# Performance work log

Measured on AMD Instinct MI355X. Metric: run time of the kernel, lower is better.

The kernel has to match this reference:

```python
import jax, jax.numpy as jnp
import numpy as np

B, T, F, H, L = 128, 256, 1024, 1024, 2

def setup_inputs() -> dict:
    key = jax.random.key(0)
    ks = jax.random.split(key, 9)
    s_in = 1.0 / np.sqrt(F)
    s_h = 1.0 / np.sqrt(H)
    return {
        "x": jax.random.normal(ks[0], (B, T, F), jnp.float32),
        "W_ih0": jax.random.normal(ks[1], (4 * H, F), jnp.float32) * s_in,
        "b_ih0": jax.random.normal(ks[2], (4 * H,), jnp.float32) * s_in,
        "W_hh0": jax.random.normal(ks[3], (4 * H, H), jnp.float32) * s_h,
        "b_hh0": jax.random.normal(ks[4], (4 * H,), jnp.float32) * s_h,
        "W_ih1": jax.random.normal(ks[5], (4 * H, H), jnp.float32) * s_h,
        "b_ih1": jax.random.normal(ks[6], (4 * H,), jnp.float32) * s_h,
        "W_hh1": jax.random.normal(ks[7], (4 * H, H), jnp.float32) * s_h,
        "b_hh1": jax.random.normal(ks[8], (4 * H,), jnp.float32) * s_h,
    }

def _cell(x_t, h, c, W_ih, b_ih, W_hh, b_hh):
    # gates: (B, 4H); chunk order i, f, g, o (matches torch .chunk(4, dim=1))
    gates = x_t @ W_ih.T + b_ih + h @ W_hh.T + b_hh
    i, f, g, o = jnp.split(gates, 4, axis=1)
    i = jax.nn.sigmoid(i)
    f = jax.nn.sigmoid(f)
    g = jnp.tanh(g)
    o = jax.nn.sigmoid(o)
    c_new = f * c + i * g
    h_new = o * jnp.tanh(c_new)
    return h_new, c_new

def reference(x, W_ih0, b_ih0, W_hh0, b_hh0, W_ih1, b_ih1, W_hh1, b_hh1):
    Bv = x.shape[0]
    z = jnp.zeros((Bv, H), x.dtype)
    init = (z, z, z, z)  # h0, c0, h1, c1

    def step(carry, x_t):
        h0, c0, h1, c1 = carry
        h0, c0 = _cell(x_t, h0, c0, W_ih0, b_ih0, W_hh0, b_hh0)
        h1, c1 = _cell(h0, h1, c1, W_ih1, b_ih1, W_hh1, b_hh1)
        return (h0, c0, h1, c1), h1

    # scan over time: xs shaped (T, B, F)
    _, ys = jax.lax.scan(step, init, jnp.swapaxes(x, 0, 1))
    return jnp.swapaxes(ys, 0, 1)  # (B, T, H)
```

## Files before the change

### kernel.cpp

```cpp
#include <hip/hip_runtime.h>

#define B_ 128
#define T_ 256
#define F_ 1024
#define H_ 1024

typedef __bf16 bf16x8 __attribute__((ext_vector_type(8)));
typedef __bf16 bf16x4 __attribute__((ext_vector_type(4)));
typedef float f32x4 __attribute__((ext_vector_type(4)));

#define WROW 2056

__device__ __forceinline__ float sigf(float v)  { return 1.0f / (1.0f + __expf(-v)); }
__device__ __forceinline__ float tanhfast(float x) { return 1.0f - 2.0f / (1.0f + __expf(2.0f * x)); }

__global__ void k_cvt(const float* __restrict__ src, __bf16* __restrict__ dst, int n) {
    int i = (blockIdx.x * 256 + threadIdx.x) * 8;
    if (i + 7 < n) {
        float4 a = *(const float4*)(src + i);
        float4 b = *(const float4*)(src + i + 4);
        bf16x8 o = { (__bf16)a.x, (__bf16)a.y, (__bf16)a.z, (__bf16)a.w,
                     (__bf16)b.x, (__bf16)b.y, (__bf16)b.z, (__bf16)b.w };
        *(bf16x8*)(dst + i) = o;
    }
}

__global__ void k_init(__bf16* h0b, __bf16* h1b, unsigned* bar) {
    int i = blockIdx.x * 256 + threadIdx.x;
    h0b[i] = (__bf16)0.0f;
    h1b[i] = (__bf16)0.0f;
    if (i < 64) bar[i] = 0u;
}

#define STEP(A0, A1, KW) do { \
    bf16x8 b0_ = *(const bf16x8*)&wB[lrow][(KW) + quad * 8]; \
    bf16x8 b1_ = *(const bf16x8*)&wB[16 + lrow][(KW) + quad * 8]; \
    acc00 = __builtin_amdgcn_mfma_f32_16x16x32_bf16(A0, b0_, acc00, 0, 0, 0); \
    acc01 = __builtin_amdgcn_mfma_f32_16x16x32_bf16(A0, b1_, acc01, 0, 0, 0); \
    acc10 = __builtin_amdgcn_mfma_f32_16x16x32_bf16(A1, b0_, acc10, 0, 0, 0); \
    acc11 = __builtin_amdgcn_mfma_f32_16x16x32_bf16(A1, b1_, acc11, 0, 0, 0); \
} while (0)

#define KLOOP_BF16(SRC, STRIDE, WBASE) do { \
    const __bf16* pa_ = (SRC) + (long)arow0 * (STRIDE) + kbase + quad * 8; \
    const __bf16* pb_ = (SRC) + (long)arow1 * (STRIDE) + kbase + quad * 8; \
    _Pragma("unroll 8") \
    for (int ks_ = 0; ks_ < 16; ++ks_) { \
        bf16x8 a0_ = *(const bf16x8*)(pa_ + ks_ * 32); \
        bf16x8 a1_ = *(const bf16x8*)(pb_ + ks_ * 32); \
        STEP(a0_, a1_, (WBASE) + kbase + ks_ * 32); \
    } \
} while (0)

#define KLOOP_F32(SRC, STRIDE, WBASE) do { \
    const float* pa_ = (SRC) + (long)arow0 * (STRIDE) + kbase + quad * 8; \
    const float* pb_ = (SRC) + (long)arow1 * (STRIDE) + kbase + quad * 8; \
    _Pragma("unroll 4") \
    for (int ks_ = 0; ks_ < 16; ++ks_) { \
        float4 va_ = *(const float4*)(pa_ + ks_ * 32); \
        float4 vb_ = *(const float4*)(pa_ + ks_ * 32 + 4); \
        float4 vc_ = *(const float4*)(pb_ + ks_ * 32); \
        float4 vd_ = *(const float4*)(pb_ + ks_ * 32 + 4); \
        bf16x8 a0_ = { (__bf16)va_.x, (__bf16)va_.y, (__bf16)va_.z, (__bf16)va_.w, \
                       (__bf16)vb_.x, (__bf16)vb_.y, (__bf16)vb_.z, (__bf16)vb_.w }; \
        bf16x8 a1_ = { (__bf16)vc_.x, (__bf16)vc_.y, (__bf16)vc_.z, (__bf16)vc_.w, \
                       (__bf16)vd_.x, (__bf16)vd_.y, (__bf16)vd_.z, (__bf16)vd_.w }; \
        STEP(a0_, a1_, (WBASE) + kbase + ks_ * 32); \
    } \
} while (0)

#define ZACC() do { \
    acc00 = (f32x4){0.f,0.f,0.f,0.f}; acc01 = (f32x4){0.f,0.f,0.f,0.f}; \
    acc10 = (f32x4){0.f,0.f,0.f,0.f}; acc11 = (f32x4){0.f,0.f,0.f,0.f}; \
} while (0)

#define EPI(MT, ACC_A, ACC_B, HW, TT, WOUT) \
    _Pragma("unroll") \
    for (int r = 0; r < 4; ++r) { \
        float v0 = (ACC_A)[r], v1 = (ACC_B)[r]; \
        float q0 = __shfl_xor(v0, 8); \
        float q1 = __shfl_xor(v1, 8); \
        float iv = (hi ? q0 : v0) + bi; \
        float fv = (hi ? v0 : q0) + bf_; \
        float gv = (hi ? q1 : v1) + bg; \
        float ov = (hi ? v1 : q1) + bo; \
        float cn = sigf(fv) * creg[MT][r] + sigf(iv) * tanhfast(gv); \
        creg[MT][r] = cn; \
        float hn = sigf(ov) * tanhfast(cn); \
        if (!hi) { \
            const int b = (wave << 5) + (MT) * 16 + (quad << 2) + r; \
            (HW)[(long)b * H_ + j0 + jj] = (__bf16)hn; \
            if (WOUT) out[((long)b * T_ + (TT)) * H_ + j0 + jj] = hn; \
        } \
    }

#define REDUCE_EPI(HW, TT, WOUT) do { \
    if (wave >= 4) { \
        red[wave - 4][lane][0] = acc00; red[wave - 4][lane][1] = acc01; \
        red[wave - 4][lane][2] = acc10; red[wave - 4][lane][3] = acc11; \
    } \
    __syncthreads(); \
    if (wave < 4) { \
        acc00 += red[wave][lane][0]; acc01 += red[wave][lane][1]; \
        acc10 += red[wave][lane][2]; acc11 += red[wave][lane][3]; \
        const float bi  = bb[jj]; \
        const float bf_ = bb[8 + jj]; \
        const float bg  = bb[16 + jj]; \
        const float bo  = bb[24 + jj]; \
        EPI(0, acc00, acc01, HW, TT, WOUT); \
        EPI(1, acc10, acc11, HW, TT, WOUT); \
    } \
} while (0)

__global__ __launch_bounds__(512, 2) void lstm_persist(
    const float* __restrict__ x,
    const float* __restrict__ Wih0, const float* __restrict__ Whh0,
    const float* __restrict__ Wih1, const float* __restrict__ Whh1,
    const float* __restrict__ bih0, const float* __restrict__ bhh0,
    const float* __restrict__ bih1, const float* __restrict__ bhh1,
    __bf16* __restrict__ h0a, __bf16* __restrict__ h0b,
    __bf16* __restrict__ h1a, __bf16* __restrict__ h1b,
    unsigned* bar, const __bf16* __restrict__ xb, float* __restrict__ out)
{
    const int cell = blockIdx.x >> 7;
    const int cidx = blockIdx.x & 127;
    const int j0   = cidx << 3;

    __shared__ __align__(16) __bf16 wB[32][WROW];
    __shared__ __align__(16) f32x4  red[4][64][4];
    __shared__ float bb[32];

    const int tid  = threadIdx.x;
    const int wave = tid >> 6;
    const int lane = tid & 63;
    const int quad = lane >> 4;
    const int lrow = lane & 15;
    const int jj   = lane & 7;
    const bool hi  = (lane & 8) != 0;

    const int kbase = (wave >> 2) << 9;
    const int arow0 = ((wave & 3) << 5) + lrow;
    const int arow1 = arow0 + 16;

    unsigned* cnt = bar;
    unsigned* gen = bar + 32;

    const float* Wih = cell ? Wih1 : Wih0;
    const float* Whh = cell ? Whh1 : Whh0;

    for (int e = tid; e < 32 * 512; e += 512) {
        int n  = e >> 9;
        int k  = (e & 511) << 2;
        int wr = ((n >> 3) << 10) + j0 + (n & 7);
        const float* src = (k < 1024) ? (Wih + (long)wr * 1024 + k)
                                      : (Whh + (long)wr * 1024 + (k - 1024));
        float4 v = *(const float4*)src;
        bf16x4 o = { (__bf16)v.x, (__bf16)v.y, (__bf16)v.z, (__bf16)v.w };
        *(bf16x4*)&wB[n][k] = o;
    }
    if (tid < 32) {
        int wr = ((tid >> 3) << 10) + j0 + (tid & 7);
        bb[tid] = cell ? (bih1[wr] + bhh1[wr]) : (bih0[wr] + bhh0[wr]);
    }
    __syncthreads();

    float creg[2][4] = {};
    f32x4 acc00, acc01, acc10, acc11;
    ZACC();

    if (cell == 0) {
        if (xb) KLOOP_BF16(xb + 0, (long)T_ * F_, 0);
        else    KLOOP_F32 (x  + 0, (long)T_ * F_, 0);
    }

    for (int p = 0; p <= T_; ++p) {
        if (cell == 0) {
            if (p < T_) {
                const int t = p;
                const __bf16* hprev = (t & 1) ? h0a : h0b;
                __bf16* hw          = (t & 1) ? h0b : h0a;
                KLOOP_BF16(hprev, H_, 1024);
                REDUCE_EPI(hw, t, false);
            }
        } else {
            if (p >= 1) {
                const int t = p - 1;
                ZACC();
                const __bf16* s0 = (t & 1) ? h0b : h0a;
                const __bf16* s1 = (t & 1) ? h1a : h1b;
                __bf16* hw       = (t & 1) ? h1b : h1a;
                KLOOP_BF16(s0, H_, 0);
                KLOOP_BF16(s1, H_, 1024);
                REDUCE_EPI(hw, t, true);
            }
        }

        if (p < T_) {
            __syncthreads();
            unsigned g = 0;
            if (tid == 0) {
                __threadfence();
                g = __hip_atomic_load(gen, __ATOMIC_RELAXED, __HIP_MEMORY_SCOPE_AGENT);
                unsigned a = __hip_atomic_fetch_add(cnt, 1u, __ATOMIC_RELAXED,
                                                    __HIP_MEMORY_SCOPE_AGENT);
                if (a == 255u) {
                    __hip_atomic_store(cnt, 0u, __ATOMIC_RELAXED, __HIP_MEMORY_SCOPE_AGENT);
                    __hip_atomic_store(gen, g + 1u, __ATOMIC_RELEASE, __HIP_MEMORY_SCOPE_AGENT);
                }
            }
            if (cell == 0) {
                ZACC();
                if (p + 1 < T_) {
                    if (xb) KLOOP_BF16(xb + (long)(p + 1) * F_, (long)T_ * F_, 0);
                    else    KLOOP_F32 (x  + (long)(p + 1) * F_, (long)T_ * F_, 0);
                }
            }
            if (tid == 0) {
                for (;;) {
                    bool done = false;
                    for (int it = 0; it < 256; ++it) {
                        if (__hip_atomic_load(gen, __ATOMIC_RELAXED,
                                              __HIP_MEMORY_SCOPE_AGENT) != g) { done = true; break; }
                        __builtin_amdgcn_s_sleep(2);
                    }
                    if (done) break;
                    if (__hip_atomic_load(gen, __ATOMIC_ACQUIRE,
                                          __HIP_MEMORY_SCOPE_AGENT) != g) break;
                }
                __builtin_amdgcn_fence(__ATOMIC_ACQUIRE, "agent");
            }
            __syncthreads();
        }
    }
}

extern "C" void kernel_launch(void* const* d_in, const int* in_sizes, int n_in,
                              void* d_out, int out_size, void* d_ws, size_t ws_size,
                              hipStream_t stream)
{
    const float* x    = (const float*)d_in[0];
    const float* Wih0 = (const float*)d_in[1];
    const float* bih0 = (const float*)d_in[2];
    const float* Whh0 = (const float*)d_in[3];
    const float* bhh0 = (const float*)d_in[4];
    const float* Wih1 = (const float*)d_in[5];
    const float* bih1 = (const float*)d_in[6];
    const float* Whh1 = (const float*)d_in[7];
    const float* bhh1 = (const float*)d_in[8];
    float* out = (float*)d_out;

    char* ws = (char*)d_ws;
    unsigned* bar = (unsigned*)ws;
    __bf16* h0a = (__bf16*)(ws + 4096);
    __bf16* h0b = (__bf16*)(ws + 4096 + (256 << 10));
    __bf16* h1a = (__bf16*)(ws + 4096 + (512 << 10));
    __bf16* h1b = (__bf16*)(ws + 4096 + (768 << 10));
    const __bf16* xb = nullptr;

    const size_t XB_OFF = 4096 + (1 << 20);
    if (ws_size >= XB_OFF + ((size_t)64 << 20)) {
        __bf16* xbw = (__bf16*)(ws + XB_OFF);
        k_cvt<<<dim3(16384), dim3(256), 0, stream>>>(x, xbw, B_ * T_ * F_);
        xb = xbw;
    }
    k_init<<<dim3(512), dim3(256), 0, stream>>>(h0b, h1b, bar);

    void* args[] = {
        (void*)&x, (void*)&Wih0, (void*)&Whh0, (void*)&Wih1, (void*)&Whh1,
        (void*)&bih0, (void*)&bhh0, (void*)&bih1, (void*)&bhh1,
        (void*)&h0a, (void*)&h0b, (void*)&h1a, (void*)&h1b,
        (void*)&bar, (void*)&xb, (void*)&out
    };
    hipError_t err = hipLaunchCooperativeKernel((const void*)lstm_persist,
                                                dim3(256), dim3(512), args, 0, stream);
    if (err != hipSuccess) {
        lstm_persist<<<dim3(256), dim3(512), 0, stream>>>(
            x, Wih0, Whh0, Wih1, Whh1, bih0, bhh0, bih1, bhh1,
            h0a, h0b, h1a, h1b, bar, xb, out);
    }
    (void)in_sizes; (void)n_in; (void)out_size;
}
```

Measured before the change: 7.381 ms.

## Software-pipeline A-operand loads in K loops and transpose reduction buffer layout

Each K loop now preloads the A-operand rows (hidden state or x) into a register ring buffer and issues the load for a later step while the MFMAs for the current step run. The goal is to hide global-memory latency on the recurrent critical path. The cross-wave reduction buffer is changed from f32x4-per-lane to a scalar layout indexed [element][lane], which should avoid LDS bank conflicts. Launch bounds drop from 2 to 1 wave-group per SIMD to leave room for the extra registers, which lowers possible occupancy, though one persistent block per CU may already be the case.

```diff
diff --git a/kernel.cpp b/kernel.cpp
--- a/kernel.cpp
+++ b/kernel.cpp
@@ -44,10 +44,20 @@
 #define KLOOP_BF16(SRC, STRIDE, WBASE) do { \
     const __bf16* pa_ = (SRC) + (long)arow0 * (STRIDE) + kbase + quad * 8; \
     const __bf16* pb_ = (SRC) + (long)arow1 * (STRIDE) + kbase + quad * 8; \
-    _Pragma("unroll 8") \
+    bf16x8 ra_[8], rb_[8]; \
+    _Pragma("unroll") \
+    for (int i_ = 0; i_ < 8; ++i_) { \
+        ra_[i_] = *(const bf16x8*)(pa_ + i_ * 32); \
+        rb_[i_] = *(const bf16x8*)(pb_ + i_ * 32); \
+    } \
+    _Pragma("unroll") \
     for (int ks_ = 0; ks_ < 16; ++ks_) { \
-        bf16x8 a0_ = *(const bf16x8*)(pa_ + ks_ * 32); \
-        bf16x8 a1_ = *(const bf16x8*)(pb_ + ks_ * 32); \
+        bf16x8 a0_ = ra_[ks_ & 7]; \
+        bf16x8 a1_ = rb_[ks_ & 7]; \
+        if (ks_ < 8) { \
+            ra_[ks_ & 7] = *(const bf16x8*)(pa_ + (ks_ + 8) * 32); \
+            rb_[ks_ & 7] = *(const bf16x8*)(pb_ + (ks_ + 8) * 32); \
+        } \
         STEP(a0_, a1_, (WBASE) + kbase + ks_ * 32); \
     } \
 } while (0)
@@ -55,12 +65,24 @@
 #define KLOOP_F32(SRC, STRIDE, WBASE) do { \
     const float* pa_ = (SRC) + (long)arow0 * (STRIDE) + kbase + quad * 8; \
     const float* pb_ = (SRC) + (long)arow1 * (STRIDE) + kbase + quad * 8; \
-    _Pragma("unroll 4") \
+    float4 rA_[4], rB_[4], rC_[4], rD_[4]; \
+    _Pragma("unroll") \
+    for (int i_ = 0; i_ < 4; ++i_) { \
+        rA_[i_] = *(const float4*)(pa_ + i_ * 32); \
+        rB_[i_] = *(const float4*)(pa_ + i_ * 32 + 4); \
+        rC_[i_] = *(const float4*)(pb_ + i_ * 32); \
+        rD_[i_] = *(const float4*)(pb_ + i_ * 32 + 4); \
+    } \
+    _Pragma("unroll") \
     for (int ks_ = 0; ks_ < 16; ++ks_) { \
-        float4 va_ = *(const float4*)(pa_ + ks_ * 32); \
-        float4 vb_ = *(const float4*)(pa_ + ks_ * 32 + 4); \
-        float4 vc_ = *(const float4*)(pb_ + ks_ * 32); \
-        float4 vd_ = *(const float4*)(pb_ + ks_ * 32 + 4); \
+        float4 va_ = rA_[ks_ & 3], vb_ = rB_[ks_ & 3]; \
+        float4 vc_ = rC_[ks_ & 3], vd_ = rD_[ks_ & 3]; \
+        if (ks_ < 12) { \
+            rA_[ks_ & 3] = *(const float4*)(pa_ + (ks_ + 4) * 32); \
+            rB_[ks_ & 3] = *(const float4*)(pa_ + (ks_ + 4) * 32 + 4); \
+            rC_[ks_ & 3] = *(const float4*)(pb_ + (ks_ + 4) * 32); \
+            rD_[ks_ & 3] = *(const float4*)(pb_ + (ks_ + 4) * 32 + 4); \
+        } \
         bf16x8 a0_ = { (__bf16)va_.x, (__bf16)va_.y, (__bf16)va_.z, (__bf16)va_.w, \
                        (__bf16)vb_.x, (__bf16)vb_.y, (__bf16)vb_.z, (__bf16)vb_.w }; \
         bf16x8 a1_ = { (__bf16)vc_.x, (__bf16)vc_.y, (__bf16)vc_.z, (__bf16)vc_.w, \
@@ -96,13 +118,23 @@
 
 #define REDUCE_EPI(HW, TT, WOUT) do { \
     if (wave >= 4) { \
-        red[wave - 4][lane][0] = acc00; red[wave - 4][lane][1] = acc01; \
-        red[wave - 4][lane][2] = acc10; red[wave - 4][lane][3] = acc11; \
+        _Pragma("unroll") \
+        for (int i_ = 0; i_ < 4; ++i_) { \
+            red[wave - 4][i_     ][lane] = acc00[i_]; \
+            red[wave - 4][i_ + 4 ][lane] = acc01[i_]; \
+            red[wave - 4][i_ + 8 ][lane] = acc10[i_]; \
+            red[wave - 4][i_ + 12][lane] = acc11[i_]; \
+        } \
     } \
     __syncthreads(); \
     if (wave < 4) { \
-        acc00 += red[wave][lane][0]; acc01 += red[wave][lane][1]; \
-        acc10 += red[wave][lane][2]; acc11 += red[wave][lane][3]; \
+        _Pragma("unroll") \
+        for (int i_ = 0; i_ < 4; ++i_) { \
+            acc00[i_] += red[wave][i_     ][lane]; \
+            acc01[i_] += red[wave][i_ + 4 ][lane]; \
+            acc10[i_] += red[wave][i_ + 8 ][lane]; \
+            acc11[i_] += red[wave][i_ + 12][lane]; \
+        } \
         const float bi  = bb[jj]; \
         const float bf_ = bb[8 + jj]; \
         const float bg  = bb[16 + jj]; \
@@ -112,7 +144,7 @@
     } \
 } while (0)
 
-__global__ __launch_bounds__(512, 2) void lstm_persist(
+__global__ __launch_bounds__(512, 1) void lstm_persist(
     const float* __restrict__ x,
     const float* __restrict__ Wih0, const float* __restrict__ Whh0,
     const float* __restrict__ Wih1, const float* __restrict__ Whh1,
@@ -127,7 +159,7 @@
     const int j0   = cidx << 3;
 
     __shared__ __align__(16) __bf16 wB[32][WROW];
-    __shared__ __align__(16) f32x4  red[4][64][4];
+    __shared__ __align__(16) float  red[4][16][64];
     __shared__ float bb[32];
 
     const int tid  = threadIdx.x;
```

Measured after the change: 7.376 ms. Within noise of the previous version (-0.1%).

## Replace global barrier with per-cell hierarchical counters and multi-slot hidden state buffers

Applied to the files above, without the earlier changes.

Replaces the single grid-wide barrier per timestep with a two-level (leaf/root) counter tree per layer and per-layer generation flags. Consumers wait only on the specific layer state they need, so layer 0 and layer 1 can run skewed in a wavefront pipeline. Hidden states go into time-indexed slots (all T slots if the workspace is large, otherwise a 4-slot ring with back-pressure) stored in a k-blocked layout for coalesced loads. The K split across waves changes from halves of one matrix to x-part versus h-part. The reduction scratch is transposed, and launch bounds drop to one block per CU. It adds memory-ordering complexity and relies on spin-waits being correct.

```diff
diff --git a/kernel.cpp b/kernel.cpp
--- a/kernel.cpp
+++ b/kernel.cpp
@@ -10,6 +10,7 @@
 typedef float f32x4 __attribute__((ext_vector_type(4)));
 
 #define WROW 2056
+#define HSLOT 131072L
 
 __device__ __forceinline__ float sigf(float v)  { return 1.0f / (1.0f + __expf(-v)); }
 __device__ __forceinline__ float tanhfast(float x) { return 1.0f - 2.0f / (1.0f + __expf(2.0f * x)); }
@@ -25,12 +26,20 @@
     }
 }
 
-__global__ void k_init(__bf16* h0b, __bf16* h1b, unsigned* bar) {
+__global__ void k_init(__bf16* h0s, __bf16* h1s, unsigned* bar) {
     int i = blockIdx.x * 256 + threadIdx.x;
-    h0b[i] = (__bf16)0.0f;
-    h1b[i] = (__bf16)0.0f;
-    if (i < 64) bar[i] = 0u;
-}
+    h0s[i] = (__bf16)0.0f;
+    h1s[i] = (__bf16)0.0f;
+    if (i < 512) bar[i] = 0u;
+}
+
+#define WAITGE(P, V) do { \
+    while (__hip_atomic_load((P), __ATOMIC_RELAXED, __HIP_MEMORY_SCOPE_AGENT) < (V)) \
+        __builtin_amdgcn_s_sleep(1); \
+    asm volatile("" ::: "memory"); \
+} while (0)
+
+#define ACQ() __builtin_amdgcn_fence(__ATOMIC_ACQUIRE, "agent")
 
 #define STEP(A0, A1, KW) do { \
     bf16x8 b0_ = *(const bf16x8*)&wB[lrow][(KW) + quad * 8]; \
@@ -41,22 +50,32 @@
     acc11 = __builtin_amdgcn_mfma_f32_16x16x32_bf16(A1, b1_, acc11, 0, 0, 0); \
 } while (0)
 
-#define KLOOP_BF16(SRC, STRIDE, WBASE) do { \
-    const __bf16* pa_ = (SRC) + (long)arow0 * (STRIDE) + kbase + quad * 8; \
-    const __bf16* pb_ = (SRC) + (long)arow1 * (STRIDE) + kbase + quad * 8; \
-    _Pragma("unroll 8") \
-    for (int ks_ = 0; ks_ < 16; ++ks_) { \
+#define KLOOP_HF(SRC, WBASE) do { \
+    const __bf16* ph_ = (SRC) + (long)quad * 1024 + arow0 * 8; \
+    _Pragma("unroll") \
+    for (int ks_ = 0; ks_ < 32; ++ks_) { \
+        bf16x8 a0_ = *(const bf16x8*)(ph_ + (long)ks_ * 4096); \
+        bf16x8 a1_ = *(const bf16x8*)(ph_ + (long)ks_ * 4096 + 128); \
+        STEP(a0_, a1_, (WBASE) + ks_ * 32); \
+    } \
+} while (0)
+
+#define KLOOP_RMF(SRC, S, WBASE) do { \
+    const __bf16* pa_ = (SRC) + (long)arow0 * (S) + quad * 8; \
+    const __bf16* pb_ = (SRC) + (long)arow1 * (S) + quad * 8; \
+    _Pragma("unroll") \
+    for (int ks_ = 0; ks_ < 32; ++ks_) { \
         bf16x8 a0_ = *(const bf16x8*)(pa_ + ks_ * 32); \
         bf16x8 a1_ = *(const bf16x8*)(pb_ + ks_ * 32); \
-        STEP(a0_, a1_, (WBASE) + kbase + ks_ * 32); \
-    } \
-} while (0)
-
-#define KLOOP_F32(SRC, STRIDE, WBASE) do { \
-    const float* pa_ = (SRC) + (long)arow0 * (STRIDE) + kbase + quad * 8; \
-    const float* pb_ = (SRC) + (long)arow1 * (STRIDE) + kbase + quad * 8; \
-    _Pragma("unroll 4") \
-    for (int ks_ = 0; ks_ < 16; ++ks_) { \
+        STEP(a0_, a1_, (WBASE) + ks_ * 32); \
+    } \
+} while (0)
+
+#define KLOOP_F32F(SRC, S, WBASE) do { \
+    const float* pa_ = (SRC) + (long)arow0 * (S) + quad * 8; \
+    const float* pb_ = (SRC) + (long)arow1 * (S) + quad * 8; \
+    _Pragma("unroll") \
+    for (int ks_ = 0; ks_ < 32; ++ks_) { \
         float4 va_ = *(const float4*)(pa_ + ks_ * 32); \
         float4 vb_ = *(const float4*)(pa_ + ks_ * 32 + 4); \
         float4 vc_ = *(const float4*)(pb_ + ks_ * 32); \
@@ -65,7 +84,7 @@
                        (__bf16)vb_.x, (__bf16)vb_.y, (__bf16)vb_.z, (__bf16)vb_.w }; \
         bf16x8 a1_ = { (__bf16)vc_.x, (__bf16)vc_.y, (__bf16)vc_.z, (__bf16)vc_.w, \
                        (__bf16)vd_.x, (__bf16)vd_.y, (__bf16)vd_.z, (__bf16)vd_.w }; \
-        STEP(a0_, a1_, (WBASE) + kbase + ks_ * 32); \
+        STEP(a0_, a1_, (WBASE) + ks_ * 32); \
     } \
 } while (0)
 
@@ -89,20 +108,30 @@
         float hn = sigf(ov) * tanhfast(cn); \
         if (!hi) { \
             const int b = (wave << 5) + (MT) * 16 + (quad << 2) + r; \
-            (HW)[(long)b * H_ + j0 + jj] = (__bf16)hn; \
+            (HW)[b * 8 + jj] = (__bf16)hn; \
             if (WOUT) out[((long)b * T_ + (TT)) * H_ + j0 + jj] = hn; \
         } \
     }
 
 #define REDUCE_EPI(HW, TT, WOUT) do { \
     if (wave >= 4) { \
-        red[wave - 4][lane][0] = acc00; red[wave - 4][lane][1] = acc01; \
-        red[wave - 4][lane][2] = acc10; red[wave - 4][lane][3] = acc11; \
+        _Pragma("unroll") \
+        for (int i_ = 0; i_ < 4; ++i_) { \
+            red[wave - 4][i_     ][lane] = acc00[i_]; \
+            red[wave - 4][i_ + 4 ][lane] = acc01[i_]; \
+            red[wave - 4][i_ + 8 ][lane] = acc10[i_]; \
+            red[wave - 4][i_ + 12][lane] = acc11[i_]; \
+        } \
     } \
     __syncthreads(); \
     if (wave < 4) { \
-        acc00 += red[wave][lane][0]; acc01 += red[wave][lane][1]; \
-        acc10 += red[wave][lane][2]; acc11 += red[wave][lane][3]; \
+        _Pragma("unroll") \
+        for (int i_ = 0; i_ < 4; ++i_) { \
+            acc00[i_] += red[wave][i_     ][lane]; \
+            acc01[i_] += red[wave][i_ + 4 ][lane]; \
+            acc10[i_] += red[wave][i_ + 8 ][lane]; \
+            acc11[i_] += red[wave][i_ + 12][lane]; \
+        } \
         const float bi  = bb[jj]; \
         const float bf_ = bb[8 + jj]; \
         const float bg  = bb[16 + jj]; \
@@ -112,22 +141,22 @@
     } \
 } while (0)
 
-__global__ __launch_bounds__(512, 2) void lstm_persist(
+__global__ __launch_bounds__(512, 1) void lstm_persist(
     const float* __restrict__ x,
     const float* __restrict__ Wih0, const float* __restrict__ Whh0,
     const float* __restrict__ Wih1, const float* __restrict__ Whh1,
     const float* __restrict__ bih0, const float* __restrict__ bhh0,
     const float* __restrict__ bih1, const float* __restrict__ bhh1,
-    __bf16* __restrict__ h0a, __bf16* __restrict__ h0b,
-    __bf16* __restrict__ h1a, __bf16* __restrict__ h1b,
-    unsigned* bar, const __bf16* __restrict__ xb, float* __restrict__ out)
+    __bf16* __restrict__ h0s, __bf16* __restrict__ h1s,
+    unsigned* bar, const __bf16* __restrict__ xb,
+    float* __restrict__ out, int big)
 {
     const int cell = blockIdx.x >> 7;
     const int cidx = blockIdx.x & 127;
     const int j0   = cidx << 3;
 
     __shared__ __align__(16) __bf16 wB[32][WROW];
-    __shared__ __align__(16) f32x4  red[4][64][4];
+    __shared__ __align__(16) float  red[4][16][64];
     __shared__ float bb[32];
 
     const int tid  = threadIdx.x;
@@ -138,12 +167,14 @@
     const int jj   = lane & 7;
     const bool hi  = (lane & 8) != 0;
 
-    const int kbase = (wave >> 2) << 9;
     const int arow0 = ((wave & 3) << 5) + lrow;
     const int arow1 = arow0 + 16;
 
-    unsigned* cnt = bar;
-    unsigned* gen = bar + 32;
+    unsigned* leaf = bar + (cell ? 160 : 0) + ((cidx & 7) << 4);
+    unsigned* root = bar + (cell ? 288 : 128);
+    unsigned* genA = bar + 144;
+    unsigned* genB = bar + 304;
+    unsigned* genMy = cell ? genB : genA;
 
     const float* Wih = cell ? Wih1 : Wih0;
     const float* Whh = cell ? Whh1 : Whh0;
@@ -166,70 +197,50 @@
 
     float creg[2][4] = {};
     f32x4 acc00, acc01, acc10, acc11;
-    ZACC();
-
-    if (cell == 0) {
-        if (xb) KLOOP_BF16(xb + 0, (long)T_ * F_, 0);
-        else    KLOOP_F32 (x  + 0, (long)T_ * F_, 0);
-    }
-
-    for (int p = 0; p <= T_; ++p) {
+
+    for (int t = 0; t < T_; ++t) {
+        const long sprev = big ? (long)t : (long)(t & 3);
+        const long scur  = big ? (long)(t + 1) : (long)((t + 1) & 3);
+        ZACC();
+
+        if (!big && cell == 0 && t >= 3) WAITGE(genB, (unsigned)(t - 3));
+
         if (cell == 0) {
-            if (p < T_) {
-                const int t = p;
-                const __bf16* hprev = (t & 1) ? h0a : h0b;
-                __bf16* hw          = (t & 1) ? h0b : h0a;
-                KLOOP_BF16(hprev, H_, 1024);
-                REDUCE_EPI(hw, t, false);
+            if (wave < 4) {
+                if (xb) KLOOP_RMF(xb + (long)t * F_, (long)T_ * F_, 0);
+                else    KLOOP_F32F(x + (long)t * F_, (long)T_ * F_, 0);
+            } else {
+                WAITGE(genA, (unsigned)t);
+                if (!big) ACQ();
+                KLOOP_HF(h0s + sprev * HSLOT, 1024);
             }
         } else {
-            if (p >= 1) {
-                const int t = p - 1;
-                ZACC();
-                const __bf16* s0 = (t & 1) ? h0b : h0a;
-                const __bf16* s1 = (t & 1) ? h1a : h1b;
-                __bf16* hw       = (t & 1) ? h1b : h1a;
-                KLOOP_BF16(s0, H_, 0);
-                KLOOP_BF16(s1, H_, 1024);
-                REDUCE_EPI(hw, t, true);
+            if (wave < 4) {
+                WAITGE(genA, (unsigned)(t + 1));
+                if (!big) ACQ();
+                KLOOP_HF(h0s + scur * HSLOT, 0);
+            } else {
+                WAITGE(genB, (unsigned)t);
+                if (!big) ACQ();
+                KLOOP_HF(h1s + sprev * HSLOT, 1024);
             }
         }
 
-        if (p < T_) {
-            __syncthreads();
-            unsigned g = 0;
-            if (tid == 0) {
-                __threadfence();
-                g = __hip_atomic_load(gen, __ATOMIC_RELAXED, __HIP_MEMORY_SCOPE_AGENT);
-                unsigned a = __hip_atomic_fetch_add(cnt, 1u, __ATOMIC_RELAXED,
-                                                    __HIP_MEMORY_SCOPE_AGENT);
-                if (a == 255u) {
-                    __hip_atomic_store(cnt, 0u, __ATOMIC_RELAXED, __HIP_MEMORY_SCOPE_AGENT);
-                    __hip_atomic_store(gen, g + 1u, __ATOMIC_RELEASE, __HIP_MEMORY_SCOPE_AGENT);
-                }
+        __bf16* hw = (cell ? h1s : h0s) + scur * HSLOT + (long)cidx * 1024;
+        REDUCE_EPI(hw, t, cell != 0);
+
+        __syncthreads();
+        if (tid == 0) {
+            __threadfence();
+            unsigned v = __hip_atomic_fetch_add(leaf, 1u, __ATOMIC_RELAXED,
+                                                __HIP_MEMORY_SCOPE_AGENT) + 1u;
+            if (v == 16u * (unsigned)(t + 1)) {
+                unsigned r = __hip_atomic_fetch_add(root, 1u, __ATOMIC_RELAXED,
+                                                    __HIP_MEMORY_SCOPE_AGENT) + 1u;
+                if (r == 8u * (unsigned)(t + 1))
+                    __hip_atomic_store(genMy, (unsigned)(t + 1),
+                                       __ATOMIC_RELEASE, __HIP_MEMORY_SCOPE_AGENT);
             }
-            if (cell == 0) {
-                ZACC();
-                if (p + 1 < T_) {
-                    if (xb) KLOOP_BF16(xb + (long)(p + 1) * F_, (long)T_ * F_, 0);
-                    else    KLOOP_F32 (x  + (long)(p + 1) * F_, (long)T_ * F_, 0);
-                }
-            }
-            if (tid == 0) {
-                for (;;) {
-                    bool done = false;
-                    for (int it = 0; it < 256; ++it) {
-                        if (__hip_atomic_load(gen, __ATOMIC_RELAXED,
-                                              __HIP_MEMORY_SCOPE_AGENT) != g) { done = true; break; }
-                        __builtin_amdgcn_s_sleep(2);
-                    }
-                    if (done) break;
-                    if (__hip_atomic_load(gen, __ATOMIC_ACQUIRE,
-                                          __HIP_MEMORY_SCOPE_AGENT) != g) break;
-                }
-                __builtin_amdgcn_fence(__ATOMIC_ACQUIRE, "agent");
-            }
-            __syncthreads();
         }
     }
 }
@@ -249,34 +260,39 @@
     const float* bhh1 = (const float*)d_in[8];
     float* out = (float*)d_out;
 
+    const size_t SLOT_B = 262144;
     char* ws = (char*)d_ws;
     unsigned* bar = (unsigned*)ws;
-    __bf16* h0a = (__bf16*)(ws + 4096);
-    __bf16* h0b = (__bf16*)(ws + 4096 + (256 << 10));
-    __bf16* h1a = (__bf16*)(ws + 4096 + (512 << 10));
-    __bf16* h1b = (__bf16*)(ws + 4096 + (768 << 10));
+
+    const size_t bigNeed = 4096 + 2 * 257 * SLOT_B + ((size_t)64 << 20);
+    const int big = (ws_size >= bigNeed) ? 1 : 0;
+    const size_t nslot = big ? 257 : 4;
+
+    __bf16* h0s = (__bf16*)(ws + 4096);
+    __bf16* h1s = (__bf16*)(ws + 4096 + nslot * SLOT_B);
+    const size_t xb_off = 4096 + 2 * nslot * SLOT_B;
     const __bf16* xb = nullptr;
 
-    const size_t XB_OFF = 4096 + (1 << 20);
-    if (ws_size >= XB_OFF + ((size_t)64 << 20)) {
-        __bf16* xbw = (__bf16*)(ws + XB_OFF);
+    if (ws_size >= xb_off + ((size_t)64 << 20)) {
+        __bf16* xbw = (__bf16*)(ws + xb_off);
         k_cvt<<<dim3(16384), dim3(256), 0, stream>>>(x, xbw, B_ * T_ * F_);
         xb = xbw;
     }
-    k_init<<<dim3(512), dim3(256), 0, stream>>>(h0b, h1b, bar);
-
+    k_init<<<dim3(512), dim3(256), 0, stream>>>(h0s, h1s, bar);
+
+    int bigv = big;
     void* args[] = {
         (void*)&x, (void*)&Wih0, (void*)&Whh0, (void*)&Wih1, (void*)&Whh1,
         (void*)&bih0, (void*)&bhh0, (void*)&bih1, (void*)&bhh1,
-        (void*)&h0a, (void*)&h0b, (void*)&h1a, (void*)&h1b,
-        (void*)&bar, (void*)&xb, (void*)&out
+        (void*)&h0s, (void*)&h1s, (void*)&bar, (void*)&xb, (void*)&out,
+        (void*)&bigv
     };
     hipError_t err = hipLaunchCooperativeKernel((const void*)lstm_persist,
                                                 dim3(256), dim3(512), args, 0, stream);
     if (err != hipSuccess) {
         lstm_persist<<<dim3(256), dim3(512), 0, stream>>>(
             x, Wih0, Whh0, Wih1, Whh1, bih0, bhh0, bih1, bhh1,
-            h0a, h0b, h1a, h1b, bar, xb, out);
+            h0s, h1s, bar, xb, out, bigv);
     }
     (void)in_sizes; (void)n_in; (void)out_size;
 }
```

Measured after the change: 5.982 ms. 19.0% less time.
